# Kernel tuning notes

Measured on AMD Instinct MI355X. Metric: run time of the kernel, lower is better.

## Reference

```python
import jax, jax.numpy as jnp
import numpy as np

B, T, D, H = 8, 512, 1024, 16
DK = D // H          # 64
S = 2 * T - 1        # 1023 relative positions


def setup_inputs() -> dict:
    key = jax.random.key(0)
    ks = jax.random.split(key, 10)
    s = 0.02
    return {
        "x": jax.random.normal(ks[0], (B, T, D), jnp.float32),
        "mask": jax.random.randint(ks[1], (B, T, T), 0, 2) > 0,
        "pos": jax.random.normal(ks[2], (1, S, D), jnp.float32),
        "Wqkv": jax.random.normal(ks[3], (3 * D, D), jnp.float32) * s,
        "bqkv": jnp.zeros((3 * D,), jnp.float32),
        "Wpos": jax.random.normal(ks[4], (D, D), jnp.float32) * s,
        "posu": jax.random.normal(ks[5], (1, 1, H, DK), jnp.float32) * s,
        "posv": jax.random.normal(ks[6], (1, 1, H, DK), jnp.float32) * s,
        "Wout": jax.random.normal(ks[7], (D, D), jnp.float32) * s,
        "bout": jnp.zeros((D,), jnp.float32),
    }


def reference(x, mask, pos, Wqkv, bqkv, Wpos, posu, posv, Wout, bout):
    # QKV projection and head split
    qkv = x @ Wqkv.T + bqkv                               # [B,T,3D]
    q, k, v = jnp.split(qkv, 3, axis=-1)
    q = q.reshape(B, T, H, DK)                            # [B,T,H,dk]
    k = k.reshape(B, T, H, DK).transpose(0, 2, 1, 3)      # [B,H,T,dk]
    v = v.reshape(B, T, H, DK).transpose(0, 2, 1, 3)      # [B,H,T,dk]
    # positional projection (no bias)
    p = (pos @ Wpos.T).reshape(1, S, H, DK).transpose(0, 2, 1, 3)  # [1,H,S,dk]
    # content (AC) and position (BD) terms
    q_u = (q + posu).transpose(0, 2, 1, 3)                # [B,H,T,dk]
    q_v = (q + posv).transpose(0, 2, 1, 3)                # [B,H,T,dk]
    AC = jnp.einsum('bhtd,bhsd->bhts', q_u, k)            # [B,H,T,T]
    matrix_bd = jnp.einsum('bhtd,zhsd->bhts', q_v, p)     # [B,H,T,S]
    # Transformer-XL style relative gather: index (j - i) + (T-1)
    r = jnp.arange(T)
    rel = (r[None, :] - r[:, None]) + (T - 1)             # [T,T], values in [0, S)
    BD = jnp.take_along_axis(matrix_bd, rel[None, None], axis=3)  # [B,H,T,T]
    scores = (AC + BD) / jnp.sqrt(jnp.float32(DK))
    scores = jnp.where(mask[:, None], scores, jnp.float32(-100000.0))
    weights = jax.nn.softmax(scores, axis=-1)             # [B,H,T,T]
    ctx = jnp.einsum('bhts,bhsd->bthd', weights, v).reshape(B, T, D)
    out = ctx @ Wout.T + bout                             # dropout rate 0 -> identity
    return out, weights
```

## Files before the change

### kernel.cpp

```cpp
#include <hip/hip_runtime.h>

#define BB 8
#define TT 512
#define DD 1024
#define HH 16
#define DKK 64
#define SS 1023

typedef unsigned short u16;
typedef __attribute__((ext_vector_type(8))) short bf16x8;
typedef __attribute__((ext_vector_type(4))) float f32x4;

#define MFMA16(a, b, c) __builtin_amdgcn_mfma_f32_16x16x32_bf16((a), (b), (c), 0, 0, 0)

#define WAVE_SYNC() do { asm volatile("s_waitcnt lgkmcnt(0)" ::: "memory"); __builtin_amdgcn_sched_barrier(0); } while (0)

__device__ __forceinline__ float us2f(u16 u) {
    unsigned int x = ((unsigned int)u) << 16;
    return __uint_as_float(x);
}
__device__ __forceinline__ u16 f2us(float f) {
    unsigned int x = __float_as_uint(f);
    unsigned int lsb = (x >> 16) & 1u;
    x += 0x7fffu + lsb;
    return (u16)(x >> 16);
}
__device__ __forceinline__ bf16x8 cvt8(const float* p) {
    float4 f1 = *(const float4*)p;
    float4 f2 = *(const float4*)(p + 4);
    bf16x8 r;
    r[0] = (short)f2us(f1.x); r[1] = (short)f2us(f1.y);
    r[2] = (short)f2us(f1.z); r[3] = (short)f2us(f1.w);
    r[4] = (short)f2us(f2.x); r[5] = (short)f2us(f2.y);
    r[6] = (short)f2us(f2.z); r[7] = (short)f2us(f2.w);
    return r;
}
__device__ __forceinline__ void gload_lds16(const u16* g, u16* l) {
    __builtin_amdgcn_global_load_lds(
        (const __attribute__((address_space(1))) void*)g,
        (__attribute__((address_space(3))) void*)l, 16, 0, 0);
}

__global__ void detect_kernel(const u16* __restrict__ w,
                              const unsigned int* __restrict__ mask,
                              int* __restrict__ flags) {
    if (threadIdx.x == 0 && blockIdx.x == 0) {
        int plaus = 0;
        for (int i = 0; i < 256; i++) {
            u16 hw = w[i];
            int e = (hw >> 7) & 0xFF;
            if (e == 0 || (e >= 87 && e <= 131)) plaus++;
        }
        flags[0] = (plaus >= 205) ? 1 : 0;
        int ok = 1;
        for (int i = 0; i < 64; i++) if (mask[i] > 1u) ok = 0;
        flags[1] = ok;
    }
}

__global__ __launch_bounds__(256) void pack_mask(const void* __restrict__ mask,
                                                 unsigned int* __restrict__ packed,
                                                 const int* __restrict__ flags) {
    const int idx = blockIdx.x * 256 + threadIdx.x;
    const int g = idx & 15;
    const size_t bt = (size_t)(idx >> 4);
    unsigned int bits = 0;
    if (flags[1]) {
        const int* mp = (const int*)mask + bt * TT + g;
        #pragma unroll
        for (int k = 0; k < 32; k++) if (mp[k * 16] != 0) bits |= (1u << k);
    } else {
        const signed char* mp = (const signed char*)mask + bt * TT + g;
        #pragma unroll
        for (int k = 0; k < 32; k++) if (mp[k * 16] != 0) bits |= (1u << k);
    }
    packed[idx] = bits;
}

__global__ __launch_bounds__(256) void cvt_bf16(const void* __restrict__ src,
                                                u16* __restrict__ dst, int n8,
                                                const int* __restrict__ flags) {
    const bool isbf = (flags[0] != 0);
    int i = blockIdx.x * 256 + threadIdx.x;
    const int stride = gridDim.x * 256;
    for (; i < n8; i += stride) {
        if (isbf)
            *(bf16x8*)(dst + (size_t)i * 8) = *(const bf16x8*)((const u16*)src + (size_t)i * 8);
        else
            *(bf16x8*)(dst + (size_t)i * 8) = cvt8((const float*)src + (size_t)i * 8);
    }
}

template<int OMODE>
__global__ __launch_bounds__(256) void gemm_mfma(
    const u16* __restrict__ A, const u16* __restrict__ Bw,
    const void* __restrict__ bias, const int* __restrict__ flags,
    float* __restrict__ qT, u16* __restrict__ kB, u16* __restrict__ vB,
    u16* __restrict__ pB, void* __restrict__ oout, int M, int N, int K)
{
    const bool isbf = (flags[0] != 0);
    __shared__ u16 As[128 * 32];
    __shared__ u16 Bs[128 * 32];
    const int tid = threadIdx.x;
    const int w = tid >> 6, lane = tid & 63;
    const int quad = lane >> 4, l16 = lane & 15;
    const int wr = w >> 1, wc = w & 1;
    const int bn = blockIdx.x * 128, bm = blockIdx.y * 128;
    const int c0 = w * 2, c1 = w * 2 + 1;
    const int sr0 = c0 * 16 + (lane >> 2);
    const int sr1 = c1 * 16 + (lane >> 2);
    const int skoff = (lane & 3) * 8;

    f32x4 acc[4][4];
    #pragma unroll
    for (int m = 0; m < 4; m++)
        #pragma unroll
        for (int n = 0; n < 4; n++) {
            acc[m][n][0] = 0.f; acc[m][n][1] = 0.f;
            acc[m][n][2] = 0.f; acc[m][n][3] = 0.f;
        }

    for (int k0 = 0; k0 < K; k0 += 32) {
        int ar0 = bm + sr0, ar1 = bm + sr1;
        if (OMODE == 1) { ar0 = min(ar0, M - 1); ar1 = min(ar1, M - 1); }
        __syncthreads();
        gload_lds16(A + (size_t)ar0 * K + k0 + skoff, As + c0 * 512);
        gload_lds16(A + (size_t)ar1 * K + k0 + skoff, As + c1 * 512);
        gload_lds16(Bw + (size_t)(bn + sr0) * K + k0 + skoff, Bs + c0 * 512);
        gload_lds16(Bw + (size_t)(bn + sr1) * K + k0 + skoff, Bs + c1 * 512);
        asm volatile("s_waitcnt vmcnt(0)" ::: "memory");
        __syncthreads();

        bf16x8 af[4], bfr[4];
        #pragma unroll
        for (int m = 0; m < 4; m++)
            af[m] = *(const bf16x8*)&As[(wr * 64 + m * 16 + l16) * 32 + quad * 8];
        #pragma unroll
        for (int n = 0; n < 4; n++)
            bfr[n] = *(const bf16x8*)&Bs[(wc * 64 + n * 16 + l16) * 32 + quad * 8];
        #pragma unroll
        for (int m = 0; m < 4; m++)
            #pragma unroll
            for (int n = 0; n < 4; n++)
                acc[m][n] = MFMA16(af[m], bfr[n], acc[m][n]);
    }

    #pragma unroll
    for (int m = 0; m < 4; m++)
        #pragma unroll
        for (int nn = 0; nn < 4; nn++)
            #pragma unroll
            for (int rr = 0; rr < 4; rr++) {
                const int i = bm + wr * 64 + m * 16 + quad * 4 + rr;
                const int n = bn + wc * 64 + nn * 16 + l16;
                float val = acc[m][nn][rr];
                if (OMODE == 0) {
                    val += isbf ? us2f(((const u16*)bias)[n]) : ((const float*)bias)[n];
                    const int sec = n >> 10, w_ = n & 1023;
                    const int h_ = w_ >> 6, d_ = w_ & 63;
                    const size_t bh_ = (size_t)((i >> 9) * HH + h_);
                    const int t_ = i & 511;
                    if (sec == 0) qT[((bh_ * TT + t_) << 6) + d_] = val;
                    else if (sec == 1) kB[((bh_ * TT + t_) << 6) + d_] = f2us(val);
                    else vB[((bh_ * DKK + d_) << 9) + t_] = f2us(val);
                } else if (OMODE == 1) {
                    if (i < M) {
                        const int h_ = n >> 6, d_ = n & 63;
                        pB[((size_t)(h_ * 1024 + i) << 6) + d_] = f2us(val);
                    }
                } else {
                    val += isbf ? us2f(((const u16*)bias)[n]) : ((const float*)bias)[n];
                    if (isbf) ((u16*)oout)[(size_t)i * N + n] = f2us(val);
                    else ((float*)oout)[(size_t)i * N + n] = val;
                }
            }
}

__global__ __launch_bounds__(256) void attn_mfma(
    float* __restrict__ qT, const u16* __restrict__ kB, const u16* __restrict__ vB,
    const u16* __restrict__ pB, const void* __restrict__ posu,
    const void* __restrict__ posv, const unsigned int* __restrict__ pmask,
    void* __restrict__ d_out, u16* __restrict__ ctxB, const int* __restrict__ flags)
{
    const int b = blockIdx.x;
    const int h = blockIdx.y;
    const int t0 = blockIdx.z << 6;
    const int tid = threadIdx.x;
    const int w = tid >> 6, lane = tid & 63;
    const int quad = lane >> 4, l16 = lane & 15;
    const bool isbf = (flags[0] != 0);
    const size_t bh = (size_t)b * HH + h;

    __shared__ u16 wls[4][16][268];
    u16* wme = &wls[w][0][0];
    float* bdw = (float*)wme;

    const int trow = t0 + w * 16 + quad * 4;
    unsigned int mrow[4];
    #pragma unroll
    for (int r = 0; r < 4; r++)
        mrow[r] = pmask[((size_t)(b * TT + trow + r) << 4) + l16];

    const int myrow = t0 + w * 16 + l16;
    const float* qrow = qT + ((bh * TT + myrow) << 6);
    bf16x8 aU[2], aV[2];
    #pragma unroll
    for (int f = 0; f < 2; f++) {
        const int d0 = f * 32 + quad * 8;
        float q8[8], pu8[8], pv8[8];
        *(float4*)&q8[0] = *(const float4*)(qrow + d0);
        *(float4*)&q8[4] = *(const float4*)(qrow + d0 + 4);
        if (isbf) {
            const u16* puP = (const u16*)posu + h * 64 + d0;
            const u16* pvP = (const u16*)posv + h * 64 + d0;
            #pragma unroll
            for (int j = 0; j < 8; j++) { pu8[j] = us2f(puP[j]); pv8[j] = us2f(pvP[j]); }
        } else {
            const float* puP = (const float*)posu + h * 64 + d0;
            const float* pvP = (const float*)posv + h * 64 + d0;
            #pragma unroll
            for (int j = 0; j < 8; j++) { pu8[j] = puP[j]; pv8[j] = pvP[j]; }
        }
        #pragma unroll
        for (int j = 0; j < 8; j++) {
            aU[f][j] = (short)f2us((q8[j] + pu8[j]) * 0.125f);
            aV[f][j] = (short)f2us((q8[j] + pv8[j]) * 0.125f);
        }
    }

    f32x4 S[32];
    #pragma unroll
    for (int ct = 0; ct < 32; ct++) { S[ct][0] = 0.f; S[ct][1] = 0.f; S[ct][2] = 0.f; S[ct][3] = 0.f; }
    const u16* kbase = kB + ((bh * TT) << 6) + quad * 8;
    #pragma unroll
    for (int ct = 0; ct < 32; ct++) {
        const u16* kp = kbase + ((size_t)(ct * 16 + l16) << 6);
        bf16x8 b0 = *(const bf16x8*)kp;
        bf16x8 b1 = *(const bf16x8*)(kp + 32);
        S[ct] = MFMA16(aU[0], b0, S[ct]);
        S[ct] = MFMA16(aU[1], b1, S[ct]);
    }

    const u16* pbaseh = pB + ((size_t)h << 16);
    for (int g = 0; g < 8; g++) {
        const int pb = g * 64 - t0 + 496 - w * 16;
        #pragma unroll
        for (int c5 = 0; c5 < 5; c5++) {
            const u16* pp = pbaseh + ((size_t)(pb + c5 * 16 + l16) << 6) + quad * 8;
            bf16x8 b0 = *(const bf16x8*)pp;
            bf16x8 b1 = *(const bf16x8*)(pp + 32);
            f32x4 c; c[0] = 0.f; c[1] = 0.f; c[2] = 0.f; c[3] = 0.f;
            c = MFMA16(aV[0], b0, c);
            c = MFMA16(aV[1], b1, c);
            #pragma unroll
            for (int r = 0; r < 4; r++)
                bdw[(quad * 4 + r) * 84 + c5 * 16 + l16] = c[r];
        }
        WAVE_SYNC();
        #pragma unroll
        for (int f = 0; f < 4; f++) {
            const int sc = f * 16 + l16;
            #pragma unroll
            for (int r = 0; r < 4; r++) {
                const int local = quad * 4 + r;
                S[g * 4 + f][r] += bdw[local * 83 + sc + 15];
            }
        }
    }

    #pragma unroll
    for (int ct = 0; ct < 32; ct++) {
        #pragma unroll
        for (int r = 0; r < 4; r++) {
            if (!(mrow[r] & (1u << ct))) S[ct][r] = -100000.0f;
        }
    }

    float mx[4] = {-3.0e38f, -3.0e38f, -3.0e38f, -3.0e38f};
    float sm[4] = {0.f, 0.f, 0.f, 0.f};
    #pragma unroll
    for (int ct = 0; ct < 32; ct++)
        #pragma unroll
        for (int r = 0; r < 4; r++) mx[r] = fmaxf(mx[r], S[ct][r]);
    #pragma unroll
    for (int r = 0; r < 4; r++)
        #pragma unroll
        for (int off = 1; off < 16; off <<= 1) mx[r] = fmaxf(mx[r], __shfl_xor(mx[r], off, 64));
    #pragma unroll
    for (int ct = 0; ct < 32; ct++)
        #pragma unroll
        for (int r = 0; r < 4; r++) {
            float e = __expf(S[ct][r] - mx[r]);
            S[ct][r] = e;
            sm[r] += e;
        }
    #pragma unroll
    for (int r = 0; r < 4; r++) {
        #pragma unroll
        for (int off = 1; off < 16; off <<= 1) sm[r] += __shfl_xor(sm[r], off, 64);
        sm[r] = 1.0f / sm[r];
    }

    f32x4 Cv[4];
    #pragma unroll
    for (int i = 0; i < 4; i++) { Cv[i][0] = 0.f; Cv[i][1] = 0.f; Cv[i][2] = 0.f; Cv[i][3] = 0.f; }
    const u16* vb0 = vB + ((bh * DKK) << 9) + quad * 8;
    const size_t wbase = (size_t)BB * TT * DD + (((bh * TT + trow)) << 9) + l16;

    #pragma unroll
    for (int p = 0; p < 2; p++) {
        #pragma unroll
        for (int cl = 0; cl < 16; cl++) {
            const int ct = p * 16 + cl;
            #pragma unroll
            for (int r = 0; r < 4; r++) {
                const float wv = S[ct][r] * sm[r];
                wls[w][quad * 4 + r][cl * 16 + l16] = f2us(wv);
                if (!isbf) ((float*)d_out)[wbase + ((size_t)r << 9) + ct * 16] = wv;
            }
        }
        WAVE_SYNC();
        if (isbf) {
            u16* wout = (u16*)d_out + (size_t)BB * TT * DD + ((bh * TT + t0 + w * 16) << 9) + p * 256;
            const int sr = lane >> 5, sc8 = (lane & 31) * 8;
            #pragma unroll
            for (int rr = 0; rr < 8; rr++) {
                bf16x8 vv = *(const bf16x8*)&wls[w][rr * 2 + sr][sc8];
                *(bf16x8*)(wout + ((size_t)(rr * 2 + sr) << 9) + sc8) = vv;
            }
        }
        #pragma unroll
        for (int kl = 0; kl < 8; kl++) {
            const int ks = p * 8 + kl;
            bf16x8 aw = *(const bf16x8*)&wls[w][l16][kl * 32 + quad * 8];
            #pragma unroll
            for (int ctd = 0; ctd < 4; ctd++) {
                const u16* vp = vb0 + ((size_t)(ctd * 16 + l16) << 9) + ks * 32;
                bf16x8 bv = *(const bf16x8*)vp;
                Cv[ctd] = MFMA16(aw, bv, Cv[ctd]);
            }
        }
        WAVE_SYNC();
    }

    u16* crow = ctxB + ((size_t)(b * TT + trow) << 10) + h * 64 + l16;
    #pragma unroll
    for (int ctd = 0; ctd < 4; ctd++)
        #pragma unroll
        for (int r = 0; r < 4; r++)
            crow[((size_t)r << 10) + ctd * 16] = f2us(Cv[ctd][r]);
}

extern "C" void kernel_launch(void* const* d_in, const int* in_sizes, int n_in,
                              void* d_out, int out_size, void* d_ws, size_t ws_size,
                              hipStream_t stream)
{
    const void* x    = d_in[0];
    const void* mask = d_in[1];
    const void* pos  = d_in[2];
    const void* Wqkv = d_in[3];
    const void* bqkv = d_in[4];
    const void* Wpos = d_in[5];
    const void* posu = d_in[6];
    const void* posv = d_in[7];
    const void* Wout = d_in[8];
    const void* bout = d_in[9];

    char* ws = (char*)d_ws;
    float* qT    = (float*)(ws + 0);
    u16*   kB    = (u16*)(ws + 16777216);
    u16*   vB    = (u16*)(ws + 25165824);
    u16*   pB    = (u16*)(ws + 33554432);
    int*   flags = (int*)(ws + 35651584);
    unsigned int* pmask = (unsigned int*)(ws + 35655680);
    u16*   xB    = (u16*)(ws + 35917824);
    u16*   WqkvB = (u16*)(ws + 44306432);
    u16*   WposB = (u16*)(ws + 50597888);
    u16*   posB  = (u16*)(ws + 52695040);
    u16*   WoutB = (u16*)(ws + 54792192);
    u16*   ctxB  = xB;

    detect_kernel<<<1, 64, 0, stream>>>((const u16*)Wqkv, (const unsigned int*)mask, flags);
    pack_mask<<<dim3(256), 256, 0, stream>>>(mask, pmask, flags);

    cvt_bf16<<<dim3(1024), 256, 0, stream>>>(x,    xB,    4096 * 1024 / 8, flags);
    cvt_bf16<<<dim3(1024), 256, 0, stream>>>(Wqkv, WqkvB, 3072 * 1024 / 8, flags);
    cvt_bf16<<<dim3(512),  256, 0, stream>>>(Wpos, WposB, 1024 * 1024 / 8, flags);
    cvt_bf16<<<dim3(512),  256, 0, stream>>>(pos,  posB,  1023 * 1024 / 8, flags);
    cvt_bf16<<<dim3(512),  256, 0, stream>>>(Wout, WoutB, 1024 * 1024 / 8, flags);

    gemm_mfma<0><<<dim3(24, 32), 256, 0, stream>>>(
        xB, WqkvB, bqkv, flags, qT, kB, vB, pB, nullptr, BB * TT, 3 * DD, DD);

    gemm_mfma<1><<<dim3(8, 8), 256, 0, stream>>>(
        posB, WposB, nullptr, flags, qT, kB, vB, pB, nullptr, SS, DD, DD);

    attn_mfma<<<dim3(BB, HH, 8), 256, 0, stream>>>(
        qT, kB, vB, pB, posu, posv, pmask, d_out, ctxB, flags);

    gemm_mfma<2><<<dim3(8, 32), 256, 0, stream>>>(
        ctxB, WoutB, bout, flags, qT, kB, vB, pB, d_out, BB * TT, DD, DD);
}
```

Before: 442.7 us.

## Double-buffer GEMM LDS tiles and merge bf16 conversion launches into one kernel

The GEMM kernel now keeps two LDS stages for the A and B tiles. It issues the global-to-LDS loads for the next K slice before running the MFMAs on the current one, so memory latency overlaps with compute and one barrier per iteration goes away. The five separate fp32-to-bf16 conversion launches are merged into a single grid-stride kernel that dispatches on a flat index, which removes launch overhead and tail gaps. The cost is double the LDS per block, which may lower occupancy, plus some branching in the merged conversion loop.

```diff
diff --git a/kernel.cpp b/kernel.cpp
--- a/kernel.cpp
+++ b/kernel.cpp
@@ -77,17 +77,33 @@
     packed[idx] = bits;
 }
 
-__global__ __launch_bounds__(256) void cvt_bf16(const void* __restrict__ src,
-                                                u16* __restrict__ dst, int n8,
-                                                const int* __restrict__ flags) {
+__global__ __launch_bounds__(256) void cvt_all(
+    const void* __restrict__ s0, u16* __restrict__ d0, int n0,
+    const void* __restrict__ s1, u16* __restrict__ d1, int n1,
+    const void* __restrict__ s2, u16* __restrict__ d2, int n2,
+    const void* __restrict__ s3, u16* __restrict__ d3, int n3,
+    const void* __restrict__ s4, u16* __restrict__ d4, int n4,
+    const int* __restrict__ flags)
+{
     const bool isbf = (flags[0] != 0);
-    int i = blockIdx.x * 256 + threadIdx.x;
-    const int stride = gridDim.x * 256;
-    for (; i < n8; i += stride) {
+    const int total = n0 + n1 + n2 + n3 + n4;
+    for (int i = blockIdx.x * 256 + threadIdx.x; i < total; i += gridDim.x * 256) {
+        const void* s; u16* d; int j = i;
+        if (j < n0) { s = s0; d = d0; }
+        else { j -= n0;
+            if (j < n1) { s = s1; d = d1; }
+            else { j -= n1;
+                if (j < n2) { s = s2; d = d2; }
+                else { j -= n2;
+                    if (j < n3) { s = s3; d = d3; }
+                    else { j -= n3; s = s4; d = d4; }
+                }
+            }
+        }
         if (isbf)
-            *(bf16x8*)(dst + (size_t)i * 8) = *(const bf16x8*)((const u16*)src + (size_t)i * 8);
+            *(bf16x8*)(d + (size_t)j * 8) = *(const bf16x8*)((const u16*)s + (size_t)j * 8);
         else
-            *(bf16x8*)(dst + (size_t)i * 8) = cvt8((const float*)src + (size_t)i * 8);
+            *(bf16x8*)(d + (size_t)j * 8) = cvt8((const float*)s + (size_t)j * 8);
     }
 }
 
@@ -99,16 +115,19 @@
     u16* __restrict__ pB, void* __restrict__ oout, int M, int N, int K)
 {
     const bool isbf = (flags[0] != 0);
-    __shared__ u16 As[128 * 32];
-    __shared__ u16 Bs[128 * 32];
+    __shared__ u16 As[2][128 * 32];
+    __shared__ u16 Bs[2][128 * 32];
     const int tid = threadIdx.x;
     const int w = tid >> 6, lane = tid & 63;
     const int quad = lane >> 4, l16 = lane & 15;
     const int wr = w >> 1, wc = w & 1;
     const int bn = blockIdx.x * 128, bm = blockIdx.y * 128;
     const int c0 = w * 2, c1 = w * 2 + 1;
-    const int sr0 = c0 * 16 + (lane >> 2);
-    const int sr1 = c1 * 16 + (lane >> 2);
+    int ar0 = bm + c0 * 16 + (lane >> 2);
+    int ar1 = bm + c1 * 16 + (lane >> 2);
+    if (OMODE == 1) { ar0 = min(ar0, M - 1); ar1 = min(ar1, M - 1); }
+    const int br0 = bn + c0 * 16 + (lane >> 2);
+    const int br1 = bn + c1 * 16 + (lane >> 2);
     const int skoff = (lane & 3) * 8;
 
     f32x4 acc[4][4];
@@ -120,29 +139,40 @@
             acc[m][n][2] = 0.f; acc[m][n][3] = 0.f;
         }
 
-    for (int k0 = 0; k0 < K; k0 += 32) {
-        int ar0 = bm + sr0, ar1 = bm + sr1;
-        if (OMODE == 1) { ar0 = min(ar0, M - 1); ar1 = min(ar1, M - 1); }
-        __syncthreads();
-        gload_lds16(A + (size_t)ar0 * K + k0 + skoff, As + c0 * 512);
-        gload_lds16(A + (size_t)ar1 * K + k0 + skoff, As + c1 * 512);
-        gload_lds16(Bw + (size_t)(bn + sr0) * K + k0 + skoff, Bs + c0 * 512);
-        gload_lds16(Bw + (size_t)(bn + sr1) * K + k0 + skoff, Bs + c1 * 512);
-        asm volatile("s_waitcnt vmcnt(0)" ::: "memory");
-        __syncthreads();
-
+    gload_lds16(A + (size_t)ar0 * K + skoff, &As[0][c0 * 512]);
+    gload_lds16(A + (size_t)ar1 * K + skoff, &As[0][c1 * 512]);
+    gload_lds16(Bw + (size_t)br0 * K + skoff, &Bs[0][c0 * 512]);
+    gload_lds16(Bw + (size_t)br1 * K + skoff, &Bs[0][c1 * 512]);
+    asm volatile("s_waitcnt vmcnt(0)" ::: "memory");
+    __syncthreads();
+
+    const int nt = K >> 5;
+    int cur = 0;
+    for (int t = 0; t < nt; ++t) {
+        if (t + 1 < nt) {
+            const int kn = (t + 1) << 5;
+            gload_lds16(A + (size_t)ar0 * K + kn + skoff, &As[cur ^ 1][c0 * 512]);
+            gload_lds16(A + (size_t)ar1 * K + kn + skoff, &As[cur ^ 1][c1 * 512]);
+            gload_lds16(Bw + (size_t)br0 * K + kn + skoff, &Bs[cur ^ 1][c0 * 512]);
+            gload_lds16(Bw + (size_t)br1 * K + kn + skoff, &Bs[cur ^ 1][c1 * 512]);
+        }
         bf16x8 af[4], bfr[4];
         #pragma unroll
         for (int m = 0; m < 4; m++)
-            af[m] = *(const bf16x8*)&As[(wr * 64 + m * 16 + l16) * 32 + quad * 8];
+            af[m] = *(const bf16x8*)&As[cur][(wr * 64 + m * 16 + l16) * 32 + quad * 8];
         #pragma unroll
         for (int n = 0; n < 4; n++)
-            bfr[n] = *(const bf16x8*)&Bs[(wc * 64 + n * 16 + l16) * 32 + quad * 8];
+            bfr[n] = *(const bf16x8*)&Bs[cur][(wc * 64 + n * 16 + l16) * 32 + quad * 8];
         #pragma unroll
         for (int m = 0; m < 4; m++)
             #pragma unroll
             for (int n = 0; n < 4; n++)
                 acc[m][n] = MFMA16(af[m], bfr[n], acc[m][n]);
+        if (t + 1 < nt) {
+            asm volatile("s_waitcnt vmcnt(0)" ::: "memory");
+            __syncthreads();
+            cur ^= 1;
+        }
     }
 
     #pragma unroll
@@ -383,11 +413,13 @@
     detect_kernel<<<1, 64, 0, stream>>>((const u16*)Wqkv, (const unsigned int*)mask, flags);
     pack_mask<<<dim3(256), 256, 0, stream>>>(mask, pmask, flags);
 
-    cvt_bf16<<<dim3(1024), 256, 0, stream>>>(x,    xB,    4096 * 1024 / 8, flags);
-    cvt_bf16<<<dim3(1024), 256, 0, stream>>>(Wqkv, WqkvB, 3072 * 1024 / 8, flags);
-    cvt_bf16<<<dim3(512),  256, 0, stream>>>(Wpos, WposB, 1024 * 1024 / 8, flags);
-    cvt_bf16<<<dim3(512),  256, 0, stream>>>(pos,  posB,  1023 * 1024 / 8, flags);
-    cvt_bf16<<<dim3(512),  256, 0, stream>>>(Wout, WoutB, 1024 * 1024 / 8, flags);
+    cvt_all<<<dim3(2048), 256, 0, stream>>>(
+        x, xB, 4096 * 1024 / 8,
+        Wqkv, WqkvB, 3072 * 1024 / 8,
+        Wpos, WposB, 1024 * 1024 / 8,
+        pos, posB, 1023 * 1024 / 8,
+        Wout, WoutB, 1024 * 1024 / 8,
+        flags);
 
     gemm_mfma<0><<<dim3(24, 32), 256, 0, stream>>>(
         xB, WqkvB, bqkv, flags, qT, kB, vB, pB, nullptr, BB * TT, 3 * DD, DD);
```

Measured after the change: 434.2 us (median of 2 runs). Within noise of the previous version (-1.9%).
